# Kernel tuning notes

Hardware: AMD Instinct MI355X
Metric: run time of the kernel (lower is better)

## Reference

```python
import jax, jax.numpy as jnp
import numpy as np

B, T, C = 2, 2048, 2048
NH, NKV = 16, 16
HD = C // NH            # 128
GATE_CH = 32
ROPE_BASE = 10000.0


def setup_inputs() -> dict:
    key = jax.random.key(0)
    ks = jax.random.split(key, 8)
    x = jax.random.normal(ks[0], (B, T, C), jnp.float32)
    ve = jax.random.normal(ks[1], (B, T, C), jnp.float32)
    # RoPE tables: half-dim rotation, shape broadcastable to [B, T, H, HD//2]
    d2 = HD // 2
    inv_freq = 1.0 / (ROPE_BASE ** (jnp.arange(d2, dtype=jnp.float32) / d2))
    angles = jnp.arange(T, dtype=jnp.float32)[:, None] * inv_freq[None, :]  # [T, d2]
    cos = jnp.cos(angles)[None, :, None, :]  # [1, T, 1, d2]
    sin = jnp.sin(angles)[None, :, None, :]
    s = 0.02
    Wq = jax.random.normal(ks[2], (C, NH * HD), jnp.float32) * s
    Wk = jax.random.normal(ks[3], (C, NKV * HD), jnp.float32) * s
    Wv = jax.random.normal(ks[4], (C, NKV * HD), jnp.float32) * s
    Wgate = jax.random.normal(ks[5], (GATE_CH, NKV), jnp.float32) * s
    Wproj = jax.random.normal(ks[6], (NH * HD, C), jnp.float32) * s
    return {"x": x, "ve": ve, "cos": cos, "sin": sin,
            "Wq": Wq, "Wk": Wk, "Wv": Wv, "Wgate": Wgate, "Wproj": Wproj}


def _apply_rotary(x, cos, sin):
    d = x.shape[3] // 2
    x1, x2 = x[..., :d], x[..., d:]
    return jnp.concatenate([x1 * cos + x2 * sin, x1 * -sin + x2 * cos], axis=3)


def _rms_norm(x):
    return x * jax.lax.rsqrt(jnp.mean(x * x, axis=-1, keepdims=True) + 1e-6)


def reference(x, ve, cos, sin, Wq, Wk, Wv, Wgate, Wproj):
    b, t, c = x.shape
    q = (x @ Wq).reshape(b, t, NH, HD)
    k = (x @ Wk).reshape(b, t, NKV, HD)
    v = (x @ Wv).reshape(b, t, NKV, HD)
    # value-embedding gate
    ve_r = ve.reshape(b, t, NKV, HD)
    gate = 2.0 * jax.nn.sigmoid(x[..., :GATE_CH] @ Wgate)  # [B, T, NKV]
    v = v + gate[..., None] * ve_r
    # RoPE then QK-RMSNorm
    q = _rms_norm(_apply_rotary(q, cos, sin))
    k = _rms_norm(_apply_rotary(k, cos, sin))
    # causal attention, scale = 1/sqrt(head_dim)
    scale = 1.0 / np.sqrt(HD).astype(np.float32)
    scores = jnp.einsum('bqhd,bkhd->bhqk', q, k) * scale
    causal = jnp.tril(jnp.ones((t, t), dtype=bool))
    scores = jnp.where(causal, scores, jnp.finfo(scores.dtype).min)
    probs = jax.nn.softmax(scores, axis=-1)
    y = jnp.einsum('bhqk,bkhd->bqhd', probs, v)
    y = y.reshape(b, t, NH * HD)
    return y @ Wproj
```

## Files before the change

### kernel.cpp

```cpp
#include <hip/hip_runtime.h>
#include <stdint.h>

typedef short bf16x8 __attribute__((ext_vector_type(8)));
typedef float f32x4 __attribute__((ext_vector_type(4)));

#define ASYNC16(g, l) __builtin_amdgcn_global_load_lds( \
    (const __attribute__((address_space(1))) unsigned int*)(g), \
    (__attribute__((address_space(3))) unsigned int*)(l), 16, 0, 0)

__device__ __forceinline__ float bf2f(short u) {
  union { unsigned int i; float f; } v;
  v.i = ((unsigned int)(unsigned short)u) << 16;
  return v.f;
}
__device__ __forceinline__ short f2bf(float f) {
  union { float f; unsigned int i; } v;
  v.f = f;
  return (short)(unsigned short)((v.i + 0x8000u) >> 16);
}
__device__ __forceinline__ float ldf(const void* p, long i, int isbf) {
  return isbf ? bf2f(((const short*)p)[i]) : ((const float*)p)[i];
}

__global__ void detect_dtype(const short* __restrict__ x, int* __restrict__ flag) {
  if (threadIdx.x == 0 && blockIdx.x == 0) {
    int cnt = 0;
    for (int i = 0; i < 128; ++i) {
      int e = (((unsigned short)x[i]) >> 7) & 0xFF;
      if (e >= 110 && e <= 136) ++cnt;
    }
    *flag = (cnt >= 120) ? 1 : 0;
  }
}

__global__ __launch_bounds__(256) void convert_x(
    const void* __restrict__ xin, short* __restrict__ xb, const int* __restrict__ flag) {
  long i = (long)blockIdx.x * 2048 + (long)threadIdx.x * 8;
  if (*flag) {
    *(bf16x8*)(xb + i) = *(const bf16x8*)((const short*)xin + i);
  } else {
    const float* xf = (const float*)xin;
    short tmp[8];
    #pragma unroll
    for (int j = 0; j < 8; ++j) tmp[j] = f2bf(xf[i + j]);
    *(bf16x8*)(xb + i) = *(bf16x8*)tmp;
  }
}

__global__ __launch_bounds__(256) void transpose_w(
    const void* __restrict__ S0, short* __restrict__ D0,
    const void* __restrict__ S1, short* __restrict__ D1,
    const void* __restrict__ S2, short* __restrict__ D2,
    const int* __restrict__ flag)
{
  int z = blockIdx.z;
  const void* S = (z == 0) ? S0 : (z == 1) ? S1 : S2;
  short* D = (z == 0) ? D0 : (z == 1) ? D1 : D2;
  int isbf = *flag;
  __shared__ short tile[32][33];
  int c0 = blockIdx.x * 32, r0 = blockIdx.y * 32;
  int tx = threadIdx.x, ty = threadIdx.y;
  #pragma unroll
  for (int i = 0; i < 4; ++i)
    tile[ty + 8*i][tx] = f2bf(ldf(S, (long)(r0 + ty + 8*i) * 2048 + c0 + tx, isbf));
  __syncthreads();
  #pragma unroll
  for (int i = 0; i < 4; ++i)
    D[(long)(c0 + ty + 8*i) * 2048 + r0 + tx] = tile[tx][ty + 8*i];
}

__global__ __launch_bounds__(256) void transpose_v(
    const short* __restrict__ Vr, short* __restrict__ Vt)
{
  __shared__ short tile[32][33];
  int bh = blockIdx.z;
  int b = bh >> 4, h = bh & 15;
  int t0 = blockIdx.x * 32, d0 = blockIdx.y * 32;
  int tx = threadIdx.x, ty = threadIdx.y;
  #pragma unroll
  for (int i = 0; i < 4; ++i)
    tile[ty + 8*i][tx] = Vr[(long)(b*2048 + t0 + ty + 8*i) * 2048 + h*128 + d0 + tx];
  __syncthreads();
  #pragma unroll
  for (int i = 0; i < 4; ++i)
    Vt[((long)bh * 128 + d0 + ty + 8*i) * 2048 + t0 + tx] = tile[tx][ty + 8*i];
}

template<typename OutT>
__global__ __launch_bounds__(512, 2) void gemm_bt(
    const short* __restrict__ A,
    const short* __restrict__ B0, const short* __restrict__ B1, const short* __restrict__ B2,
    OutT* __restrict__ C0, OutT* __restrict__ C1, OutT* __restrict__ C2,
    int M, int N, int K)
{
  int z = blockIdx.z;
  const short* Bt = (z == 0) ? B0 : (z == 1) ? B1 : B2;
  OutT* C = (z == 0) ? C0 : (z == 1) ? C1 : C2;

  int m0 = blockIdx.y * 128, n0 = blockIdx.x * 256;
  int tid = threadIdx.x;
  int lane = tid & 63, w = tid >> 6;
  int quad = lane >> 4, l16 = lane & 15;
  int wm = w >> 2, wn = w & 3;

  __shared__ short As[3][128*64];
  __shared__ short Bs[3][256*64];

  f32x4 zero4 = {0.f, 0.f, 0.f, 0.f};
  f32x4 acc[4][4];
  #pragma unroll
  for (int i = 0; i < 4; ++i)
    #pragma unroll
    for (int j = 0; j < 4; ++j) acc[i][j] = zero4;

  int r8 = lane >> 3;
  int oct = (lane & 7) ^ r8;
  const short* Ab = A  + (long)(m0 + w*16 + r8) * K + oct*8;
  const short* Bb = Bt + (long)(n0 + w*32 + r8) * K + oct*8;

  int NT = K >> 6;

  #pragma unroll
  for (int u = 0; u < 2; ++u) ASYNC16(Ab + (long)u*8*K,      &As[0][(w*16 + u*8)*64]);
  #pragma unroll
  for (int u = 0; u < 4; ++u) ASYNC16(Bb + (long)u*8*K,      &Bs[0][(w*32 + u*8)*64]);
  #pragma unroll
  for (int u = 0; u < 2; ++u) ASYNC16(Ab + 64 + (long)u*8*K, &As[1][(w*16 + u*8)*64]);
  #pragma unroll
  for (int u = 0; u < 4; ++u) ASYNC16(Bb + 64 + (long)u*8*K, &Bs[1][(w*32 + u*8)*64]);
  asm volatile("s_waitcnt vmcnt(6)" ::: "memory");
  __builtin_amdgcn_s_barrier();

  int buf = 0, sbuf = 2;
  int po0 = ((0*4 + quad) ^ (l16 & 7)) * 8;
  int po1 = ((1*4 + quad) ^ (l16 & 7)) * 8;

  for (int t = 0; t < NT; ++t) {
    long ks = (long)(t + 2) * 64;
    bool st = (t + 2 < NT);

    bf16x8 a0[4], b0[4];
    #pragma unroll
    for (int i = 0; i < 4; ++i)
      a0[i] = *(const bf16x8*)&As[buf][(wm*64 + i*16 + l16)*64 + po0];
    #pragma unroll
    for (int j = 0; j < 4; ++j)
      b0[j] = *(const bf16x8*)&Bs[buf][(wn*64 + j*16 + l16)*64 + po0];
    if (st) {
      #pragma unroll
      for (int u = 0; u < 2; ++u) ASYNC16(Ab + ks + (long)u*8*K, &As[sbuf][(w*16 + u*8)*64]);
      #pragma unroll
      for (int u = 0; u < 2; ++u) ASYNC16(Bb + ks + (long)u*8*K, &Bs[sbuf][(w*32 + u*8)*64]);
    }
    __builtin_amdgcn_s_barrier();
    __builtin_amdgcn_s_setprio(1);
    #pragma unroll
    for (int i = 0; i < 4; ++i)
      #pragma unroll
      for (int j = 0; j < 4; ++j)
        acc[i][j] = __builtin_amdgcn_mfma_f32_16x16x32_bf16(a0[i], b0[j], acc[i][j], 0, 0, 0);
    __builtin_amdgcn_s_setprio(0);
    __builtin_amdgcn_s_barrier();

    bf16x8 a1[4], b1[4];
    #pragma unroll
    for (int i = 0; i < 4; ++i)
      a1[i] = *(const bf16x8*)&As[buf][(wm*64 + i*16 + l16)*64 + po1];
    #pragma unroll
    for (int j = 0; j < 4; ++j)
      b1[j] = *(const bf16x8*)&Bs[buf][(wn*64 + j*16 + l16)*64 + po1];
    if (st) {
      #pragma unroll
      for (int u = 2; u < 4; ++u) ASYNC16(Bb + ks + (long)u*8*K, &Bs[sbuf][(w*32 + u*8)*64]);
    }
    __builtin_amdgcn_s_barrier();
    __builtin_amdgcn_s_setprio(1);
    #pragma unroll
    for (int i = 0; i < 4; ++i)
      #pragma unroll
      for (int j = 0; j < 4; ++j)
        acc[i][j] = __builtin_amdgcn_mfma_f32_16x16x32_bf16(a1[i], b1[j], acc[i][j], 0, 0, 0);
    __builtin_amdgcn_s_setprio(0);
    if (t + 1 < NT) {
      if (st) asm volatile("s_waitcnt vmcnt(6)" ::: "memory");
      else    asm volatile("s_waitcnt vmcnt(0)" ::: "memory");
      __builtin_amdgcn_s_barrier();
    }
    buf  = (buf  == 2) ? 0 : buf  + 1;
    sbuf = (sbuf == 2) ? 0 : sbuf + 1;
  }

  #pragma unroll
  for (int i = 0; i < 4; ++i)
    #pragma unroll
    for (int j = 0; j < 4; ++j) {
      int row = m0 + wm*64 + i*16 + quad*4;
      int col = n0 + wn*64 + j*16 + l16;
      #pragma unroll
      for (int r = 0; r < 4; ++r) {
        float v = acc[i][j][r];
        if constexpr (sizeof(OutT) == 4)
          C[(long)(row + r) * N + col] = v;
        else
          C[(long)(row + r) * N + col] = (OutT)f2bf(v);
      }
    }
}

__global__ __launch_bounds__(256) void pointwise(
    const short* __restrict__ xb, const void* __restrict__ ve,
    const void* __restrict__ cosb, const void* __restrict__ sinb,
    const void* __restrict__ Wg, const int* __restrict__ flag,
    short* __restrict__ Qr, short* __restrict__ Kr, short* __restrict__ Vr)
{
  int row = blockIdx.x;
  int tid = threadIdx.x;
  int isbf = *flag;
  __shared__ float xg[32];
  __shared__ float gates[16];
  if (tid < 32) xg[tid] = bf2f(xb[(long)row * 2048 + tid]);
  __syncthreads();
  if (tid < 16) {
    float g = 0.f;
    #pragma unroll
    for (int i = 0; i < 32; ++i) g += xg[i] * ldf(Wg, i*16 + tid, isbf);
    gates[tid] = 2.0f / (1.0f + __expf(-g));
  }
  __syncthreads();
  #pragma unroll
  for (int it = 0; it < 8; ++it) {
    int idx = it * 256 + tid;
    int h = idx >> 7;
    long p = (long)row * 2048 + idx;
    Vr[p] = f2bf(bf2f(Vr[p]) + gates[h] * ldf(ve, p, isbf));
  }
  int lane = tid & 63, w = tid >> 6;
  int t = row & 2047;
  #pragma unroll
  for (int it = 0; it < 8; ++it) {
    int unit = it * 4 + w;
    short* P = (unit < 16) ? Qr : Kr;
    int h = unit & 15;
    long base = (long)row * 2048 + h * 128;
    float x1 = bf2f(P[base + lane]);
    float x2 = bf2f(P[base + lane + 64]);
    float c = ldf(cosb, t*64 + lane, isbf);
    float s = ldf(sinb, t*64 + lane, isbf);
    float r1 = x1 * c + x2 * s;
    float r2 = -x1 * s + x2 * c;
    float ss = r1*r1 + r2*r2;
    #pragma unroll
    for (int off = 32; off; off >>= 1) ss += __shfl_xor(ss, off);
    float rn = rsqrtf(ss * (1.0f/128.0f) + 1e-6f);
    P[base + lane]      = f2bf(r1 * rn);
    P[base + lane + 64] = f2bf(r2 * rn);
  }
}

#define FL_C1 0.12751741f
#define FL_C2 16.321698f

__global__ __launch_bounds__(256) void flash(
    const short* __restrict__ Q, const short* __restrict__ K,
    const short* __restrict__ Vt, short* __restrict__ Y)
{
  int bx = blockIdx.x;
  int bh = blockIdx.y;
  int b = bh >> 4, h = bh & 15;
  int tid = threadIdx.x;
  int lane = tid & 63, w = tid >> 6;
  int quad = lane >> 4, l16 = lane & 15;

  __shared__ short Ks[2][64*128];
  __shared__ short Vts[2][128*64];
  __shared__ short Ps[4][16*72];

  int qtA = bx, qtB = 31 - bx;
  int nA = qtA + 1, nB = qtB + 1;
  int total = nA + nB;

  int kkey = tid >> 4;
  int klo  = (tid & 15) ^ (kkey & 7);
  int vd   = tid >> 3;
  int vlo  = (tid & 7) ^ (vd & 7);
  const short* Kbase = K + (long)(b*2048 + kkey) * 2048 + h*128 + klo*8;
  const short* Vbase = Vt + ((long)bh*128 + vd) * 2048 + vlo*8;

  f32x4 zero4 = {0.f, 0.f, 0.f, 0.f};
  f32x4 o[8];
  float l_i[4];
  bf16x8 qf[4];
  bf16x8 ones;
  #pragma unroll
  for (int j = 0; j < 8; ++j) ones[j] = (short)0x3F80;

  auto stage = [&](int tt, int bufp) {
    int tl = (tt < nA) ? tt : tt - nA;
    long ko = (long)tl * 64 * 2048;
    int  vo = tl * 64;
    #pragma unroll
    for (int i = 0; i < 4; ++i)
      ASYNC16(Kbase + ko + (long)i*16*2048, &Ks[bufp][(i*16 + w*4)*128]);
    #pragma unroll
    for (int i = 0; i < 4; ++i)
      ASYNC16(Vbase + vo + (long)i*32*2048, &Vts[bufp][(i*32 + w*8)*64]);
  };
  auto loadQ = [&](int qt) {
    const short* Qb = Q + (long)(b*2048 + qt*64 + w*16 + l16) * 2048 + h*128;
    #pragma unroll
    for (int kt = 0; kt < 4; ++kt)
      qf[kt] = *(const bf16x8*)(Qb + kt*32 + quad*8);
  };
  auto flushO = [&](int qt) {
    #pragma unroll
    for (int r = 0; r < 4; ++r) {
      float inv = 1.0f / fmaxf(l_i[r], 1e-30f);
      short* yp = Y + (long)(b*2048 + qt*64 + w*16 + quad*4 + r) * 2048 + h*128;
      #pragma unroll
      for (int c8 = 0; c8 < 8; ++c8)
        yp[c8*16 + l16] = f2bf(o[c8][r] * inv);
    }
  };

  #pragma unroll
  for (int c = 0; c < 8; ++c) o[c] = zero4;
  #pragma unroll
  for (int r = 0; r < 4; ++r) l_i[r] = 0.f;
  loadQ(qtA);
  stage(0, 0);

  int qt = qtA, n_seg = nA, segbase = 0;
  for (int tt = 0; tt < total; ++tt) {
    int buf = tt & 1;
    asm volatile("s_waitcnt vmcnt(0)" ::: "memory");
    __builtin_amdgcn_s_barrier();
    if (tt + 1 < total) stage(tt + 1, buf ^ 1);
    if (tt == nA) {
      flushO(qtA);
      loadQ(qtB);
      #pragma unroll
      for (int c = 0; c < 8; ++c) o[c] = zero4;
      #pragma unroll
      for (int r = 0; r < 4; ++r) l_i[r] = 0.f;
      qt = qtB; n_seg = nB; segbase = nA;
    }
    int tloc = tt - segbase;
    int kv0 = tloc * 64;

    f32x4 s[4];
    __builtin_amdgcn_s_setprio(1);
    #pragma unroll
    for (int c = 0; c < 4; ++c) {
      f32x4 acc = zero4;
      #pragma unroll
      for (int kt = 0; kt < 4; ++kt) {
        int po = ((kt*4 + quad) ^ (l16 & 7)) * 8;
        bf16x8 kf = *(const bf16x8*)&Ks[buf][(c*16 + l16)*128 + po];
        acc = __builtin_amdgcn_mfma_f32_16x16x32_bf16(qf[kt], kf, acc, 0, 0, 0);
      }
      s[c] = acc;
    }
    __builtin_amdgcn_s_setprio(0);

    bool domask = (tloc == n_seg - 1);
    int qgb = qt*64 + w*16 + quad*4;
    #pragma unroll
    for (int c = 0; c < 4; ++c) {
      int kg = kv0 + c*16 + l16;
      #pragma unroll
      for (int r = 0; r < 4; ++r) {
        float t = s[c][r] * FL_C1 - FL_C2;
        if (domask && kg > qgb + r) t = -1000.0f;
        float pv = exp2f(t);
        Ps[w][(quad*4 + r)*72 + c*16 + l16] = f2bf(pv);
      }
    }
    asm volatile("s_waitcnt lgkmcnt(0)" ::: "memory");
    bf16x8 pa0 = *(const bf16x8*)&Ps[w][l16*72 + quad*8];
    bf16x8 pa1 = *(const bf16x8*)&Ps[w][l16*72 + 32 + quad*8];

    __builtin_amdgcn_s_setprio(1);
    f32x4 racc = __builtin_amdgcn_mfma_f32_16x16x32_bf16(pa0, ones, zero4, 0, 0, 0);
    racc = __builtin_amdgcn_mfma_f32_16x16x32_bf16(pa1, ones, racc, 0, 0, 0);
    #pragma unroll
    for (int r = 0; r < 4; ++r) l_i[r] += racc[r];

    #pragma unroll
    for (int c8 = 0; c8 < 8; ++c8) {
      int po0 = ((0*4 + quad) ^ (l16 & 7)) * 8;
      int po1 = ((1*4 + quad) ^ (l16 & 7)) * 8;
      bf16x8 v0 = *(const bf16x8*)&Vts[buf][(c8*16 + l16)*64 + po0];
      bf16x8 v1 = *(const bf16x8*)&Vts[buf][(c8*16 + l16)*64 + po1];
      o[c8] = __builtin_amdgcn_mfma_f32_16x16x32_bf16(pa0, v0, o[c8], 0, 0, 0);
      o[c8] = __builtin_amdgcn_mfma_f32_16x16x32_bf16(pa1, v1, o[c8], 0, 0, 0);
    }
    __builtin_amdgcn_s_setprio(0);
  }
  flushO(qtB);
}

extern "C" void kernel_launch(void* const* d_in, const int* in_sizes, int n_in,
                              void* d_out, int out_size, void* d_ws, size_t ws_size,
                              hipStream_t stream) {
  const void* x    = d_in[0];
  const void* ve   = d_in[1];
  const void* cosb = d_in[2];
  const void* sinb = d_in[3];
  const void* Wq   = d_in[4];
  const void* Wk   = d_in[5];
  const void* Wv   = d_in[6];
  const void* Wg   = d_in[7];
  const void* Wp   = d_in[8];
  float* out = (float*)d_out;

  int*   flag = (int*)d_ws;
  short* base = (short*)d_ws + 256;
  short* wt0 = base;
  short* wtk = base + 4194304L;
  short* wtv = base + 8388608L;
  short* Vt  = base + 4194304L;
  short* xb  = base + 12582912L;
  short* Y   = base + 12582912L;
  short* Qr  = base + 20971520L;
  short* Kr  = base + 29360128L;
  short* Vr  = base + 37748736L;

  detect_dtype<<<1, 64, 0, stream>>>((const short*)x, flag);
  convert_x<<<4096, 256, 0, stream>>>(x, xb, flag);
  transpose_w<<<dim3(64, 64, 3), dim3(32, 8), 0, stream>>>(Wq, wt0, Wk, wtk, Wv, wtv, flag);
  gemm_bt<short><<<dim3(8, 32, 3), 512, 0, stream>>>(xb, wt0, wtk, wtv, Qr, Kr, Vr, 4096, 2048, 2048);
  transpose_w<<<dim3(64, 64, 1), dim3(32, 8), 0, stream>>>(Wp, wt0, Wp, wt0, Wp, wt0, flag);
  pointwise<<<dim3(4096), 256, 0, stream>>>(xb, ve, cosb, sinb, Wg, flag, Qr, Kr, Vr);
  transpose_v<<<dim3(64, 4, 32), dim3(32, 8), 0, stream>>>(Vr, Vt);
  flash<<<dim3(16, 32), 256, 0, stream>>>(Qr, Kr, Vt, Y);
  gemm_bt<float><<<dim3(8, 32, 1), 512, 0, stream>>>(Y, wt0, wt0, wt0, out, out, out, 4096, 2048, 2048);
}
```

Baseline: 466.3 us.

## Enlarge GEMM tile to 256x256 with double-buffered four-phase MFMA pipeline

The bf16 GEMM kernel now computes a 256x256 output tile per block instead of 128x256. Each warp holds 8x4 accumulators, and the kernel drops from triple to double buffering in LDS. The k-loop is split into four phases that interleave async loads of the next A and B halves with MFMA bursts. The aim is more arithmetic per byte loaded, in exchange for higher register pressure, fewer blocks on the grid (which may underfill the CUs), and a full vmcnt(0) wait each iteration.

Result: slower. 495.9 us (+6.3%).

```diff
diff --git a/kernel.cpp b/kernel.cpp
--- a/kernel.cpp
+++ b/kernel.cpp
@@ -97,108 +97,130 @@
   const short* Bt = (z == 0) ? B0 : (z == 1) ? B1 : B2;
   OutT* C = (z == 0) ? C0 : (z == 1) ? C1 : C2;
 
-  int m0 = blockIdx.y * 128, n0 = blockIdx.x * 256;
+  int m0 = blockIdx.y * 256, n0 = blockIdx.x * 256;
   int tid = threadIdx.x;
   int lane = tid & 63, w = tid >> 6;
   int quad = lane >> 4, l16 = lane & 15;
   int wm = w >> 2, wn = w & 3;
 
-  __shared__ short As[3][128*64];
-  __shared__ short Bs[3][256*64];
+  __shared__ short As[2][256*64];
+  __shared__ short Bs[2][256*64];
 
   f32x4 zero4 = {0.f, 0.f, 0.f, 0.f};
-  f32x4 acc[4][4];
-  #pragma unroll
-  for (int i = 0; i < 4; ++i)
+  f32x4 acc[8][4];
+  #pragma unroll
+  for (int i = 0; i < 8; ++i)
     #pragma unroll
     for (int j = 0; j < 4; ++j) acc[i][j] = zero4;
 
   int r8 = lane >> 3;
   int oct = (lane & 7) ^ r8;
   const short* Ab = A  + (long)(m0 + w*16 + r8) * K + oct*8;
-  const short* Bb = Bt + (long)(n0 + w*32 + r8) * K + oct*8;
+  const short* Bb = Bt + (long)(n0 + w*16 + r8) * K + oct*8;
 
   int NT = K >> 6;
-
-  #pragma unroll
-  for (int u = 0; u < 2; ++u) ASYNC16(Ab + (long)u*8*K,      &As[0][(w*16 + u*8)*64]);
-  #pragma unroll
-  for (int u = 0; u < 4; ++u) ASYNC16(Bb + (long)u*8*K,      &Bs[0][(w*32 + u*8)*64]);
-  #pragma unroll
-  for (int u = 0; u < 2; ++u) ASYNC16(Ab + 64 + (long)u*8*K, &As[1][(w*16 + u*8)*64]);
-  #pragma unroll
-  for (int u = 0; u < 4; ++u) ASYNC16(Bb + 64 + (long)u*8*K, &Bs[1][(w*32 + u*8)*64]);
-  asm volatile("s_waitcnt vmcnt(6)" ::: "memory");
-  __builtin_amdgcn_s_barrier();
-
-  int buf = 0, sbuf = 2;
   int po0 = ((0*4 + quad) ^ (l16 & 7)) * 8;
   int po1 = ((1*4 + quad) ^ (l16 & 7)) * 8;
 
+  auto stA = [&](int sb, int h, long kn) {
+    #pragma unroll
+    for (int i = 0; i < 2; ++i)
+      ASYNC16(Ab + (long)(h*128 + i*8) * K + kn, &As[sb][(h*128 + w*16 + i*8)*64]);
+  };
+  auto stB = [&](int sb, int h, long kn) {
+    #pragma unroll
+    for (int i = 0; i < 2; ++i)
+      ASYNC16(Bb + (long)(h*128 + i*8) * K + kn, &Bs[sb][(h*128 + w*16 + i*8)*64]);
+  };
+
+  stA(0, 0, 0); stA(0, 1, 0); stB(0, 0, 0); stB(0, 1, 0);
+  asm volatile("s_waitcnt vmcnt(0)" ::: "memory");
+  __builtin_amdgcn_s_barrier();
+
+  bf16x8 am[8], bn0, bn1;
+
   for (int t = 0; t < NT; ++t) {
-    long ks = (long)(t + 2) * 64;
-    bool st = (t + 2 < NT);
-
-    bf16x8 a0[4], b0[4];
-    #pragma unroll
-    for (int i = 0; i < 4; ++i)
-      a0[i] = *(const bf16x8*)&As[buf][(wm*64 + i*16 + l16)*64 + po0];
-    #pragma unroll
-    for (int j = 0; j < 4; ++j)
-      b0[j] = *(const bf16x8*)&Bs[buf][(wn*64 + j*16 + l16)*64 + po0];
+    int b = t & 1, sb = b ^ 1;
+    long kn = (long)(t + 1) * 64;
+    bool st = (t + 1 < NT);
+    const short* Asb = &As[b][0];
+    const short* Bsb = &Bs[b][0];
+
+    #pragma unroll
+    for (int mf = 0; mf < 8; ++mf)
+      am[mf] = *(const bf16x8*)&Asb[(wm*128 + mf*16 + l16)*64 + po0];
+    bn0 = *(const bf16x8*)&Bsb[(wn*64 +  0 + l16)*64 + po0];
+    bn1 = *(const bf16x8*)&Bsb[(wn*64 + 16 + l16)*64 + po0];
+    if (st) stA(sb, 0, kn);
+    __builtin_amdgcn_s_barrier();
+    __builtin_amdgcn_s_setprio(1);
+    #pragma unroll
+    for (int mf = 0; mf < 8; ++mf)
+      acc[mf][0] = __builtin_amdgcn_mfma_f32_16x16x32_bf16(am[mf], bn0, acc[mf][0], 0, 0, 0);
+    #pragma unroll
+    for (int mf = 0; mf < 8; ++mf)
+      acc[mf][1] = __builtin_amdgcn_mfma_f32_16x16x32_bf16(am[mf], bn1, acc[mf][1], 0, 0, 0);
+    __builtin_amdgcn_s_setprio(0);
+    __builtin_amdgcn_s_barrier();
+
+    bn0 = *(const bf16x8*)&Bsb[(wn*64 + 32 + l16)*64 + po0];
+    bn1 = *(const bf16x8*)&Bsb[(wn*64 + 48 + l16)*64 + po0];
+    if (st) stA(sb, 1, kn);
+    __builtin_amdgcn_s_barrier();
+    __builtin_amdgcn_s_setprio(1);
+    #pragma unroll
+    for (int mf = 0; mf < 8; ++mf)
+      acc[mf][2] = __builtin_amdgcn_mfma_f32_16x16x32_bf16(am[mf], bn0, acc[mf][2], 0, 0, 0);
+    #pragma unroll
+    for (int mf = 0; mf < 8; ++mf)
+      acc[mf][3] = __builtin_amdgcn_mfma_f32_16x16x32_bf16(am[mf], bn1, acc[mf][3], 0, 0, 0);
+    __builtin_amdgcn_s_setprio(0);
+    __builtin_amdgcn_s_barrier();
+
+    #pragma unroll
+    for (int mf = 0; mf < 8; ++mf)
+      am[mf] = *(const bf16x8*)&Asb[(wm*128 + mf*16 + l16)*64 + po1];
+    bn0 = *(const bf16x8*)&Bsb[(wn*64 +  0 + l16)*64 + po1];
+    bn1 = *(const bf16x8*)&Bsb[(wn*64 + 16 + l16)*64 + po1];
+    if (st) stB(sb, 0, kn);
+    __builtin_amdgcn_s_barrier();
+    __builtin_amdgcn_s_setprio(1);
+    #pragma unroll
+    for (int mf = 0; mf < 8; ++mf)
+      acc[mf][0] = __builtin_amdgcn_mfma_f32_16x16x32_bf16(am[mf], bn0, acc[mf][0], 0, 0, 0);
+    #pragma unroll
+    for (int mf = 0; mf < 8; ++mf)
+      acc[mf][1] = __builtin_amdgcn_mfma_f32_16x16x32_bf16(am[mf], bn1, acc[mf][1], 0, 0, 0);
+    __builtin_amdgcn_s_setprio(0);
+    __builtin_amdgcn_s_barrier();
+
+    bn0 = *(const bf16x8*)&Bsb[(wn*64 + 32 + l16)*64 + po1];
+    bn1 = *(const bf16x8*)&Bsb[(wn*64 + 48 + l16)*64 + po1];
+    if (st) stB(sb, 1, kn);
+    __builtin_amdgcn_s_barrier();
+    __builtin_amdgcn_s_setprio(1);
+    #pragma unroll
+    for (int mf = 0; mf < 8; ++mf)
+      acc[mf][2] = __builtin_amdgcn_mfma_f32_16x16x32_bf16(am[mf], bn0, acc[mf][2], 0, 0, 0);
+    #pragma unroll
+    for (int mf = 0; mf < 8; ++mf)
+      acc[mf][3] = __builtin_amdgcn_mfma_f32_16x16x32_bf16(am[mf], bn1, acc[mf][3], 0, 0, 0);
+    __builtin_amdgcn_s_setprio(0);
     if (st) {
-      #pragma unroll
-      for (int u = 0; u < 2; ++u) ASYNC16(Ab + ks + (long)u*8*K, &As[sbuf][(w*16 + u*8)*64]);
-      #pragma unroll
-      for (int u = 0; u < 2; ++u) ASYNC16(Bb + ks + (long)u*8*K, &Bs[sbuf][(w*32 + u*8)*64]);
-    }
-    __builtin_amdgcn_s_barrier();
-    __builtin_amdgcn_s_setprio(1);
-    #pragma unroll
-    for (int i = 0; i < 4; ++i)
-      #pragma unroll
-      for (int j = 0; j < 4; ++j)
-        acc[i][j] = __builtin_amdgcn_mfma_f32_16x16x32_bf16(a0[i], b0[j], acc[i][j], 0, 0, 0);
-    __builtin_amdgcn_s_setprio(0);
-    __builtin_amdgcn_s_barrier();
-
-    bf16x8 a1[4], b1[4];
-    #pragma unroll
-    for (int i = 0; i < 4; ++i)
-      a1[i] = *(const bf16x8*)&As[buf][(wm*64 + i*16 + l16)*64 + po1];
-    #pragma unroll
-    for (int j = 0; j < 4; ++j)
-      b1[j] = *(const bf16x8*)&Bs[buf][(wn*64 + j*16 + l16)*64 + po1];
-    if (st) {
-      #pragma unroll
-      for (int u = 2; u < 4; ++u) ASYNC16(Bb + ks + (long)u*8*K, &Bs[sbuf][(w*32 + u*8)*64]);
-    }
-    __builtin_amdgcn_s_barrier();
-    __builtin_amdgcn_s_setprio(1);
-    #pragma unroll
-    for (int i = 0; i < 4; ++i)
-      #pragma unroll
-      for (int j = 0; j < 4; ++j)
-        acc[i][j] = __builtin_amdgcn_mfma_f32_16x16x32_bf16(a1[i], b1[j], acc[i][j], 0, 0, 0);
-    __builtin_amdgcn_s_setprio(0);
-    if (t + 1 < NT) {
-      if (st) asm volatile("s_waitcnt vmcnt(6)" ::: "memory");
-      else    asm volatile("s_waitcnt vmcnt(0)" ::: "memory");
+      asm volatile("s_waitcnt vmcnt(0)" ::: "memory");
       __builtin_amdgcn_s_barrier();
     }
-    buf  = (buf  == 2) ? 0 : buf  + 1;
-    sbuf = (sbuf == 2) ? 0 : sbuf + 1;
-  }
-
-  #pragma unroll
-  for (int i = 0; i < 4; ++i)
-    #pragma unroll
-    for (int j = 0; j < 4; ++j) {
-      int row = m0 + wm*64 + i*16 + quad*4;
-      int col = n0 + wn*64 + j*16 + l16;
+  }
+
+  #pragma unroll
+  for (int mf = 0; mf < 8; ++mf)
+    #pragma unroll
+    for (int nf = 0; nf < 4; ++nf) {
+      int row = m0 + wm*128 + mf*16 + quad*4;
+      int col = n0 + wn*64 + nf*16 + l16;
       #pragma unroll
       for (int r = 0; r < 4; ++r) {
-        float v = acc[i][j][r];
+        float v = acc[mf][nf][r];
         if constexpr (sizeof(OutT) == 4)
           C[(long)(row + r) * N + col] = v;
         else
@@ -428,10 +450,10 @@
   detect_dtype<<<1, 64, 0, stream>>>((const short*)x, flag);
   convert_x<<<4096, 256, 0, stream>>>(x, xb, flag);
   transpose_w<<<dim3(64, 64, 3), dim3(32, 8), 0, stream>>>(Wq, wt0, Wk, wtk, Wv, wtv, flag);
-  gemm_bt<short><<<dim3(8, 32, 3), 512, 0, stream>>>(xb, wt0, wtk, wtv, Qr, Kr, Vr, 4096, 2048, 2048);
+  gemm_bt<short><<<dim3(8, 16, 3), 512, 0, stream>>>(xb, wt0, wtk, wtv, Qr, Kr, Vr, 4096, 2048, 2048);
   transpose_w<<<dim3(64, 64, 1), dim3(32, 8), 0, stream>>>(Wp, wt0, Wp, wt0, Wp, wt0, flag);
   pointwise<<<dim3(4096), 256, 0, stream>>>(xb, ve, cosb, sinb, Wg, flag, Qr, Kr, Vr);
   transpose_v<<<dim3(64, 4, 32), dim3(32, 8), 0, stream>>>(Vr, Vt);
   flash<<<dim3(16, 32), 256, 0, stream>>>(Qr, Kr, Vt, Y);
-  gemm_bt<float><<<dim3(8, 32, 1), 512, 0, stream>>>(Y, wt0, wt0, wt0, out, out, out, 4096, 2048, 2048);
-}
+  gemm_bt<float><<<dim3(8, 16, 1), 512, 0, stream>>>(Y, wt0, wt0, wt0, out, out, out, 4096, 2048, 2048);
+}
```
